# Performance work log

Hardware: AMD Instinct MI355X
Metric: run time of the kernel (lower is better)

The kernel has to match this reference:

```python
import jax, jax.numpy as jnp
import numpy as np

N_NODES = 50000
N_EDGES = 800000
F_IN = 128
HIDDEN = 96
N_CLASS = 40


def setup_inputs() -> dict:
    key = jax.random.key(0)
    ks = jax.random.split(key, 16)
    x = jax.random.normal(ks[0], (N_NODES, F_IN), dtype=jnp.float32)
    edge_index = jax.random.randint(ks[1], (2, N_EDGES), 0, N_NODES, dtype=jnp.int64)
    edge_weight = jax.random.uniform(ks[2], (N_EDGES,), dtype=jnp.float32)
    s = 0.1
    return {
        "x": x,
        "edge_index": edge_index,
        "edge_weight": edge_weight,
        "W_conv1": jax.random.normal(ks[3], (F_IN, HIDDEN), dtype=jnp.float32) * s,
        "b_conv1": jnp.zeros((HIDDEN,), dtype=jnp.float32),
        "W_conv2": jax.random.normal(ks[4], (HIDDEN, HIDDEN), dtype=jnp.float32) * s,
        "b_conv2": jnp.zeros((HIDDEN,), dtype=jnp.float32),
        "W_conv3": jax.random.normal(ks[5], (HIDDEN, HIDDEN), dtype=jnp.float32) * s,
        "b_conv3": jnp.zeros((HIDDEN,), dtype=jnp.float32),
        "W_lin1": jax.random.normal(ks[6], (F_IN, HIDDEN), dtype=jnp.float32) * s,
        "b_lin1": jnp.zeros((HIDDEN,), dtype=jnp.float32),
        "W_lin2": jax.random.normal(ks[7], (HIDDEN, N_CLASS), dtype=jnp.float32) * s,
        "b_lin2": jnp.zeros((N_CLASS,), dtype=jnp.float32),
    }


def _gcn_norm(edge_index, edge_weight, num_nodes):
    # PyG gcn_norm: add self-loops (weight 1), symmetric deg^-1/2 normalization.
    row, col = edge_index[0], edge_index[1]
    loop = jnp.arange(num_nodes, dtype=edge_index.dtype)
    rows = jnp.concatenate([row, loop])
    cols = jnp.concatenate([col, loop])
    w = jnp.concatenate([edge_weight, jnp.ones((num_nodes,), edge_weight.dtype)])
    deg = jax.ops.segment_sum(w, cols, num_segments=num_nodes)
    dinv = jnp.where(deg > 0, jax.lax.rsqrt(deg), 0.0)
    norm = dinv[rows] * w * dinv[cols]  # [E + N]
    return rows, cols, norm


def _gcn_conv(x, rows, cols, norm, W, b, num_nodes):
    h = x @ W                                   # [N, H]
    msg = norm[:, None] * h[rows]               # gather + scale, [E+N, H]
    out = jax.ops.segment_sum(msg, cols, num_segments=num_nodes)  # scatter-add
    return out + b


def reference(x, edge_index, edge_weight, W_conv1, b_conv1, W_conv2, b_conv2,
              W_conv3, b_conv3, W_lin1, b_lin1, W_lin2, b_lin2):
    N = x.shape[0]
    rows, cols, norm = _gcn_norm(edge_index, edge_weight, N)
    # x1 = elu(conv1(x)); residual branch through first_lin + stacked convs
    x1 = jax.nn.elu(_gcn_conv(x, rows, cols, norm, W_conv1, b_conv1, N))
    h = jax.nn.elu(x @ W_lin1 + b_lin1)
    # dropout p=0.5 is identity in eval mode
    h = jax.nn.elu(_gcn_conv(h, rows, cols, norm, W_conv2, b_conv2, N))
    h = jax.nn.elu(_gcn_conv(h, rows, cols, norm, W_conv3, b_conv3, N))
    h = x1 + h
    logits = h @ W_lin2 + b_lin2
    return jax.nn.log_softmax(logits, axis=-1)
```

## Files before the change

kernel.cpp:

```cpp
#include <hip/hip_runtime.h>
#include <hip/hip_bf16.h>

static __device__ __forceinline__ float elu_f(float x) {
    return x > 0.f ? x : expm1f(x);
}

static __device__ __forceinline__ ushort f2bf(float x) {
    __hip_bfloat16 h = __float2bfloat16(x);
    ushort u;
    __builtin_memcpy(&u, &h, 2);
    return u;
}

typedef short bf16x8 __attribute__((ext_vector_type(8)));
typedef float f32x4  __attribute__((ext_vector_type(4)));

static __device__ __forceinline__ void bf8_unpack(uint4 v, float* f) {
    f[0] = __uint_as_float(v.x << 16);
    f[1] = __uint_as_float(v.x & 0xffff0000u);
    f[2] = __uint_as_float(v.y << 16);
    f[3] = __uint_as_float(v.y & 0xffff0000u);
    f[4] = __uint_as_float(v.z << 16);
    f[5] = __uint_as_float(v.z & 0xffff0000u);
    f[6] = __uint_as_float(v.w << 16);
    f[7] = __uint_as_float(v.w & 0xffff0000u);
}

static __device__ __forceinline__ uint4 bf8_pack(const float* a) {
    uint4 o;
    o.x = (uint)f2bf(a[0]) | ((uint)f2bf(a[1]) << 16);
    o.y = (uint)f2bf(a[2]) | ((uint)f2bf(a[3]) << 16);
    o.z = (uint)f2bf(a[4]) | ((uint)f2bf(a[5]) << 16);
    o.w = (uint)f2bf(a[6]) | ((uint)f2bf(a[7]) << 16);
    return o;
}

__global__ void k_wprep4(const float* __restrict__ W1, const float* __restrict__ W2,
                         const float* __restrict__ W3, const float* __restrict__ W4,
                         ushort* __restrict__ T1, ushort* __restrict__ T2,
                         ushort* __restrict__ T3, ushort* __restrict__ T4,
                         int* __restrict__ bcnt) {
    const int b = blockIdx.x;
    if (b == 0) bcnt[threadIdx.x] = 0;
    const float* W; ushort* T; int K, base;
    if      (b < 48)  { W = W1; T = T1; K = 128; base = b;       }
    else if (b < 96)  { W = W2; T = T2; K = 128; base = b - 48;  }
    else if (b < 132) { W = W3; T = T3; K = 96;  base = b - 96;  }
    else              { W = W4; T = T4; K = 96;  base = b - 132; }
    const int i = base * 256 + threadIdx.x;
    const int kk = i / 96, c = i - kk * 96;
    T[c * K + kk] = f2bf(W[i]);
}

__global__ __launch_bounds__(256) void
k_bcount(const int* __restrict__ col, int* __restrict__ bcnt, int E, int bspan) {
    __shared__ int h[256];
    const int tid = threadIdx.x;
    h[tid] = 0;
    __syncthreads();
    const int e0 = blockIdx.x * 4096;
    #pragma unroll
    for (int j = 0; j < 16; ++j) {
        int e = e0 + j * 256 + tid;
        if (e < E) atomicAdd(&h[col[e] / bspan], 1);
    }
    __syncthreads();
    if (h[tid] > 0) atomicAdd(&bcnt[tid], h[tid]);
}

__global__ __launch_bounds__(256) void
k_bscan(const int* __restrict__ bcnt, int* __restrict__ bOff, int* __restrict__ bCur) {
    __shared__ int wsum[4];
    const int tid = threadIdx.x, lane = tid & 63, wid = tid >> 6;
    int v = bcnt[tid];
    int s = v;
    #pragma unroll
    for (int d = 1; d < 64; d <<= 1) {
        int t = __shfl_up(s, d);
        if (lane >= d) s += t;
    }
    if (lane == 63) wsum[wid] = s;
    __syncthreads();
    int wb = 0;
    #pragma unroll
    for (int k = 0; k < 3; ++k) if (k < wid) wb += wsum[k];
    int excl = s - v + wb;
    bOff[tid] = excl;
    bCur[tid] = excl;
    if (tid == 255) bOff[256] = excl + v;
}

__global__ __launch_bounds__(256) void
k_bscatter(const int* __restrict__ row, const int* __restrict__ col,
           const float* __restrict__ w, int* __restrict__ bCur,
           int2* __restrict__ ebuf, int* __restrict__ edst, int E, int bspan) {
    __shared__ int h[256];
    __shared__ int base[256];
    const int tid = threadIdx.x;
    h[tid] = 0;
    __syncthreads();
    const int e0 = blockIdx.x * 4096;
    int bk[16], rk[16];
    #pragma unroll
    for (int j = 0; j < 16; ++j) {
        int e = e0 + j * 256 + tid;
        if (e < E) {
            int b = col[e] / bspan;
            bk[j] = b;
            rk[j] = atomicAdd(&h[b], 1);
        }
    }
    __syncthreads();
    base[tid] = (h[tid] > 0) ? atomicAdd(&bCur[tid], h[tid]) : 0;
    __syncthreads();
    #pragma unroll
    for (int j = 0; j < 16; ++j) {
        int e = e0 + j * 256 + tid;
        if (e < E) {
            int pos = base[bk[j]] + rk[j];
            ebuf[pos] = make_int2(row[e], __float_as_int(w[e]));
            edst[pos] = col[e];
        }
    }
}

__global__ __launch_bounds__(256) void
k_csrify(const int2* __restrict__ ebuf, const int* __restrict__ edst,
         const int* __restrict__ bOff, int* __restrict__ off, float* __restrict__ dinv,
         int2* __restrict__ pairs, int N, int E, int bspan) {
    __shared__ int hist[256];
    __shared__ float degs[256];
    __shared__ int curl[256];
    __shared__ int wsum[4];
    const int tid = threadIdx.x, b = blockIdx.x;
    const int base = b * bspan;
    const int lnodes = (N - base < bspan) ? (N - base) : bspan;
    if (b == 0 && tid == 0) off[N] = E;
    if (lnodes <= 0) return;
    hist[tid] = 0;
    degs[tid] = 0.f;
    __syncthreads();
    const int e0 = bOff[b], e1 = bOff[b + 1];
    for (int e = e0 + tid; e < e1; e += 256) {
        int d = edst[e] - base;
        atomicAdd(&hist[d], 1);
        atomicAdd(&degs[d], __int_as_float(ebuf[e].y));
    }
    __syncthreads();
    const int lane = tid & 63, wid = tid >> 6;
    int v = hist[tid];
    int s = v;
    #pragma unroll
    for (int d = 1; d < 64; d <<= 1) {
        int t = __shfl_up(s, d);
        if (lane >= d) s += t;
    }
    if (lane == 63) wsum[wid] = s;
    __syncthreads();
    int wb = 0;
    #pragma unroll
    for (int k = 0; k < 3; ++k) if (k < wid) wb += wsum[k];
    int excl = s - v + wb;
    if (tid < lnodes) {
        off[base + tid] = e0 + excl;
        dinv[base + tid] = rsqrtf(1.0f + degs[tid]);
    }
    curl[tid] = excl;
    __syncthreads();
    for (int e = e0 + tid; e < e1; e += 256) {
        int d = edst[e] - base;
        int p = atomicAdd(&curl[d], 1);
        pairs[e0 + p] = ebuf[e];
    }
}

template<int K, int XBF>
__global__ __launch_bounds__(256) void
k_gemm_mfma(const void* __restrict__ Xv, const ushort* __restrict__ Wt,
            const float* __restrict__ bias, const float* __restrict__ dscale,
            void* __restrict__ outp, int N, int act, int obf16) {
    constexpr int KP = K + 8;
    __shared__ ushort XT[64 * KP];
    __shared__ ushort WT[96 * KP];
    const int tid = threadIdx.x;
    const int n0  = blockIdx.x * 64;

    #pragma unroll
    for (int i = tid; i < 96 * K / 8; i += 256) {
        const int c = i / (K / 8), q = i - c * (K / 8);
        uint4 v = reinterpret_cast<const uint4*>(Wt)[i];
        *reinterpret_cast<uint4*>(&WT[c * KP + q * 8]) = v;
    }
    if (XBF) {
        const ushort* X = (const ushort*)Xv;
        #pragma unroll
        for (int i = tid; i < 64 * K / 8; i += 256) {
            const int row = i / (K / 8), q = i - row * (K / 8);
            const int n = (n0 + row < N) ? (n0 + row) : (N - 1);
            uint4 v = *reinterpret_cast<const uint4*>(X + (size_t)n * K + q * 8);
            *reinterpret_cast<uint4*>(&XT[row * KP + q * 8]) = v;
        }
    } else {
        const float* X = (const float*)Xv;
        #pragma unroll
        for (int i = tid; i < 64 * K / 4; i += 256) {
            const int row = i / (K / 4), q = i - row * (K / 4);
            const int n = (n0 + row < N) ? (n0 + row) : (N - 1);
            float4 v = *reinterpret_cast<const float4*>(X + (size_t)n * K + q * 4);
            uint lo = (uint)f2bf(v.x) | ((uint)f2bf(v.y) << 16);
            uint hi = (uint)f2bf(v.z) | ((uint)f2bf(v.w) << 16);
            *reinterpret_cast<uint2*>(&XT[row * KP + q * 4]) = make_uint2(lo, hi);
        }
    }
    __syncthreads();

    const int lane = tid & 63;
    const int wv   = tid >> 6;
    const int r16  = lane & 15;
    const int kh   = lane >> 4;

    bf16x8 a[K / 32];
    const ushort* xbase = &XT[(wv * 16 + r16) * KP + kh * 8];
    #pragma unroll
    for (int ks = 0; ks < K / 32; ++ks)
        a[ks] = *reinterpret_cast<const bf16x8*>(xbase + ks * 32);

    f32x4 acc[6];
    #pragma unroll
    for (int ct = 0; ct < 6; ++ct) {
        f32x4 c = {0.f, 0.f, 0.f, 0.f};
        const ushort* wbase = &WT[(ct * 16 + r16) * KP + kh * 8];
        #pragma unroll
        for (int ks = 0; ks < K / 32; ++ks) {
            bf16x8 bfr = *reinterpret_cast<const bf16x8*>(wbase + ks * 32);
            c = __builtin_amdgcn_mfma_f32_16x16x32_bf16(a[ks], bfr, c, 0, 0, 0);
        }
        acc[ct] = c;
    }

    #pragma unroll
    for (int r = 0; r < 4; ++r) {
        const int n = n0 + wv * 16 + kh * 4 + r;
        if (n >= N) continue;
        const float ds = dscale ? dscale[n] : 1.f;
        #pragma unroll
        for (int ct = 0; ct < 6; ++ct) {
            const int col = ct * 16 + r16;
            float v = acc[ct][r] * ds;
            if (bias) v += bias[col];
            if (act) v = elu_f(v);
            if (obf16) ((ushort*)outp)[(size_t)n * 96 + col] = f2bf(v);
            else       ((float*)outp)[(size_t)n * 96 + col] = v;
        }
    }
}

__global__ __launch_bounds__(256) void
k_aggregate(const ushort* __restrict__ tmp, const int* __restrict__ off,
            const int2* __restrict__ pairs, const float* __restrict__ dinv,
            const float* __restrict__ bias, const ushort* __restrict__ addsrc,
            ushort* __restrict__ out, int N) {
    int t = blockIdx.x * blockDim.x + threadIdx.x;
    int n = t / 6;
    if (n >= N) return;
    const int c = (t % 6) * 16;
    const ushort* base = tmp + c;

    const float di = dinv[n];
    float f[16], acc[16];
    {
        uint4 s0 = *reinterpret_cast<const uint4*>(base + (size_t)n * 96);
        uint4 s1 = *reinterpret_cast<const uint4*>(base + (size_t)n * 96 + 8);
        bf8_unpack(s0, f);
        bf8_unpack(s1, f + 8);
        #pragma unroll
        for (int i = 0; i < 16; ++i) acc[i] = f[i];
    }

    const int e0 = off[n];
    const int e1 = off[n + 1];
    const int m  = e1 - e0;

    int2 pA, pB, pC;
    uint4 hA0, hA1, hB0, hB1, hC0, hC1;
    if (m > 0) {
        pA = pairs[e0];
        const ushort* r = base + (size_t)pA.x * 96;
        hA0 = *reinterpret_cast<const uint4*>(r);
        hA1 = *reinterpret_cast<const uint4*>(r + 8);
    }
    if (m > 1) {
        pB = pairs[e0 + 1];
        const ushort* r = base + (size_t)pB.x * 96;
        hB0 = *reinterpret_cast<const uint4*>(r);
        hB1 = *reinterpret_cast<const uint4*>(r + 8);
    }
    if (m > 2) {
        pC = pairs[e0 + 2];
        const ushort* r = base + (size_t)pC.x * 96;
        hC0 = *reinterpret_cast<const uint4*>(r);
        hC1 = *reinterpret_cast<const uint4*>(r + 8);
    }

    for (int e = e0 + 3; e < e1; ++e) {
        int2 pD = pairs[e];
        const ushort* r = base + (size_t)pD.x * 96;
        uint4 hD0 = *reinterpret_cast<const uint4*>(r);
        uint4 hD1 = *reinterpret_cast<const uint4*>(r + 8);
        float w = __int_as_float(pA.y);
        bf8_unpack(hA0, f);
        bf8_unpack(hA1, f + 8);
        #pragma unroll
        for (int i = 0; i < 16; ++i) acc[i] = fmaf(w, f[i], acc[i]);
        pA = pB; hA0 = hB0; hA1 = hB1;
        pB = pC; hB0 = hC0; hB1 = hC1;
        pC = pD; hC0 = hD0; hC1 = hD1;
    }
    if (m > 0) {
        float w = __int_as_float(pA.y);
        bf8_unpack(hA0, f); bf8_unpack(hA1, f + 8);
        #pragma unroll
        for (int i = 0; i < 16; ++i) acc[i] = fmaf(w, f[i], acc[i]);
    }
    if (m > 1) {
        float w = __int_as_float(pB.y);
        bf8_unpack(hB0, f); bf8_unpack(hB1, f + 8);
        #pragma unroll
        for (int i = 0; i < 16; ++i) acc[i] = fmaf(w, f[i], acc[i]);
    }
    if (m > 2) {
        float w = __int_as_float(pC.y);
        bf8_unpack(hC0, f); bf8_unpack(hC1, f + 8);
        #pragma unroll
        for (int i = 0; i < 16; ++i) acc[i] = fmaf(w, f[i], acc[i]);
    }

    #pragma unroll
    for (int q = 0; q < 4; ++q) {
        float4 bv = *reinterpret_cast<const float4*>(bias + c + q * 4);
        acc[q * 4 + 0] = elu_f(fmaf(di, acc[q * 4 + 0], bv.x));
        acc[q * 4 + 1] = elu_f(fmaf(di, acc[q * 4 + 1], bv.y));
        acc[q * 4 + 2] = elu_f(fmaf(di, acc[q * 4 + 2], bv.z));
        acc[q * 4 + 3] = elu_f(fmaf(di, acc[q * 4 + 3], bv.w));
    }
    if (addsrc) {
        uint4 r0 = *reinterpret_cast<const uint4*>(addsrc + (size_t)n * 96 + c);
        uint4 r1 = *reinterpret_cast<const uint4*>(addsrc + (size_t)n * 96 + c + 8);
        bf8_unpack(r0, f); bf8_unpack(r1, f + 8);
        #pragma unroll
        for (int i = 0; i < 16; ++i) acc[i] += f[i];
    }
    ushort* op = out + (size_t)n * 96 + c;
    *reinterpret_cast<uint4*>(op)     = bf8_pack(acc);
    *reinterpret_cast<uint4*>(op + 8) = bf8_pack(acc + 8);
}

__global__ __launch_bounds__(128) void
k_lin2_lsm(const ushort* __restrict__ h, const float* __restrict__ W2,
           const float* __restrict__ b2, float* __restrict__ out, int N) {
    __shared__ float hsT[96][128];
    const int tid = threadIdx.x;
    const int n0 = blockIdx.x * 128;
    const int nn = (N - n0 < 128) ? (N - n0) : 128;

    if (tid < nn) {
        const ushort* hr = h + (size_t)(n0 + tid) * 96;
        #pragma unroll
        for (int q = 0; q < 12; ++q) {
            uint4 v = *reinterpret_cast<const uint4*>(hr + q * 8);
            float f[8];
            bf8_unpack(v, f);
            #pragma unroll
            for (int j = 0; j < 8; ++j) hsT[q * 8 + j][tid] = f[j];
        }
    }
    __syncthreads();

    float acc[40];
    #pragma unroll
    for (int c = 0; c < 40; ++c) acc[c] = b2[c];
    for (int k = 0; k < 96; ++k) {
        const float hv = hsT[k][tid];
        const float* wr = W2 + k * 40;
        #pragma unroll
        for (int c = 0; c < 40; ++c) acc[c] = fmaf(hv, wr[c], acc[c]);
    }

    float m = acc[0];
    #pragma unroll
    for (int c = 1; c < 40; ++c) m = fmaxf(m, acc[c]);
    float s = 0.f;
    #pragma unroll
    for (int c = 0; c < 40; ++c) s += expf(acc[c] - m);
    const float lse = m + logf(s);

    if (tid < nn) {
        float* op = out + (size_t)(n0 + tid) * 40;
        #pragma unroll
        for (int q = 0; q < 10; ++q) {
            float4 v = make_float4(acc[q * 4 + 0] - lse, acc[q * 4 + 1] - lse,
                                   acc[q * 4 + 2] - lse, acc[q * 4 + 3] - lse);
            *reinterpret_cast<float4*>(op + q * 4) = v;
        }
    }
}


extern "C" void kernel_launch(void* const* d_in, const int* in_sizes, int n_in,
                              void* d_out, int out_size, void* d_ws, size_t ws_size,
                              hipStream_t stream) {
    const float* x   = (const float*)d_in[0];
    const int*   ei  = (const int*)d_in[1];
    const float* ew  = (const float*)d_in[2];
    const float* Wc1 = (const float*)d_in[3];
    const float* bc1 = (const float*)d_in[4];
    const float* Wc2 = (const float*)d_in[5];
    const float* bc2 = (const float*)d_in[6];
    const float* Wc3 = (const float*)d_in[7];
    const float* bc3 = (const float*)d_in[8];
    const float* Wl1 = (const float*)d_in[9];
    const float* bl1 = (const float*)d_in[10];
    const float* Wl2 = (const float*)d_in[11];
    const float* bl2 = (const float*)d_in[12];

    const int FIN = 128, HID = 96;
    const int N = in_sizes[0] / FIN;
    const int E = in_sizes[2];
    const int* row = ei;
    const int* col = ei + E;
    const int bspan = (N + 255) / 256;

    char* ws = (char*)d_ws;
    size_t o = 0;
    auto alloc = [&](size_t bytes) -> void* {
        void* p = ws + o;
        o += (bytes + 255) & ~(size_t)255;
        return p;
    };
    float*  dinv   = (float*)alloc((size_t)N * 4);
    int*    off    = (int*)  alloc((size_t)(N + 1) * 4);
    int*    bcnt   = (int*)  alloc(256 * 4);
    int*    bOff   = (int*)  alloc(257 * 4);
    int*    bCur   = (int*)  alloc(256 * 4);
    int2*   pairs  = (int2*) alloc((size_t)E * 8);
    ushort* M1     = (ushort*)alloc((size_t)N * HID * 2);
    ushort* M2     = (ushort*)alloc((size_t)N * HID * 2);
    ushort* Bb     = (ushort*)alloc((size_t)N * HID * 2);
    ushort* Cb     = (ushort*)alloc((size_t)N * HID * 2);
    ushort* Wt_c1  = (ushort*)alloc(96 * 128 * 2);
    ushort* Wt_l1  = (ushort*)alloc(96 * 128 * 2);
    ushort* Wt_c2  = (ushort*)alloc(96 * 96 * 2);
    ushort* Wt_c3  = (ushort*)alloc(96 * 96 * 2);
    int2*   ebuf   = (int2*)M1;
    int*    edst   = (int*)M2;

    const int gBkt  = (E + 4095) / 4096;
    const int nGemm = (N + 63) / 64;
    const int nAgg  = (N * 6 + 255) / 256;

    k_wprep4<<<168, 256, 0, stream>>>(Wc1, Wl1, Wc2, Wc3, Wt_c1, Wt_l1, Wt_c2, Wt_c3, bcnt);

    k_bcount<<<gBkt, 256, 0, stream>>>(col, bcnt, E, bspan);
    k_bscan<<<1, 256, 0, stream>>>(bcnt, bOff, bCur);
    k_bscatter<<<gBkt, 256, 0, stream>>>(row, col, ew, bCur, ebuf, edst, E, bspan);
    k_csrify<<<256, 256, 0, stream>>>(ebuf, edst, bOff, off, dinv, pairs, N, E, bspan);

    k_gemm_mfma<128, 0><<<nGemm, 256, 0, stream>>>(x, Wt_c1, nullptr, dinv, M1, N, 0, 1);
    k_gemm_mfma<128, 0><<<nGemm, 256, 0, stream>>>(x, Wt_l1, bl1, nullptr, Cb, N, 1, 1);

    k_aggregate<<<nAgg, 256, 0, stream>>>(M1, off, pairs, dinv, bc1, nullptr, Bb, N);

    k_gemm_mfma<96, 1><<<nGemm, 256, 0, stream>>>(Cb, Wt_c2, nullptr, dinv, M2, N, 0, 1);
    k_aggregate<<<nAgg, 256, 0, stream>>>(M2, off, pairs, dinv, bc2, nullptr, Cb, N);

    k_gemm_mfma<96, 1><<<nGemm, 256, 0, stream>>>(Cb, Wt_c3, nullptr, dinv, M1, N, 0, 1);
    k_aggregate<<<nAgg, 256, 0, stream>>>(M1, off, pairs, dinv, bc3, Bb, Cb, N);

    k_lin2_lsm<<<(N + 127) / 128, 128, 0, stream>>>(Cb, Wl2, bl2, (float*)d_out, N);
}
```

Measured before the change: 229.6 us.

## Fold bucket scan into scatter/csrify, fuse first-layer GEMMs, stage edge pairs in LDS

```diff
diff --git a/kernel.cpp b/kernel.cpp
--- a/kernel.cpp
+++ b/kernel.cpp
@@ -39,9 +39,10 @@
                          const float* __restrict__ W3, const float* __restrict__ W4,
                          ushort* __restrict__ T1, ushort* __restrict__ T2,
                          ushort* __restrict__ T3, ushort* __restrict__ T4,
-                         int* __restrict__ bcnt) {
+                         int* __restrict__ bcnt, int* __restrict__ bRes) {
     const int b = blockIdx.x;
     if (b == 0) bcnt[threadIdx.x] = 0;
+    if (b == 1) bRes[threadIdx.x] = 0;
     const float* W; ushort* T; int K, base;
     if      (b < 48)  { W = W1; T = T1; K = 128; base = b;       }
     else if (b < 96)  { W = W2; T = T2; K = 128; base = b - 48;  }
@@ -69,35 +70,17 @@
 }
 
 __global__ __launch_bounds__(256) void
-k_bscan(const int* __restrict__ bcnt, int* __restrict__ bOff, int* __restrict__ bCur) {
+k_bscatter(const int* __restrict__ row, const int* __restrict__ col,
+           const float* __restrict__ w, const int* __restrict__ bcnt,
+           int* __restrict__ bRes, int2* __restrict__ ebuf, int* __restrict__ edst,
+           int E, int bspan) {
+    __shared__ int h[256];
+    __shared__ int base[256];
+    __shared__ int sOff[256];
     __shared__ int wsum[4];
     const int tid = threadIdx.x, lane = tid & 63, wid = tid >> 6;
-    int v = bcnt[tid];
-    int s = v;
-    #pragma unroll
-    for (int d = 1; d < 64; d <<= 1) {
-        int t = __shfl_up(s, d);
-        if (lane >= d) s += t;
-    }
-    if (lane == 63) wsum[wid] = s;
-    __syncthreads();
-    int wb = 0;
-    #pragma unroll
-    for (int k = 0; k < 3; ++k) if (k < wid) wb += wsum[k];
-    int excl = s - v + wb;
-    bOff[tid] = excl;
-    bCur[tid] = excl;
-    if (tid == 255) bOff[256] = excl + v;
-}
-
-__global__ __launch_bounds__(256) void
-k_bscatter(const int* __restrict__ row, const int* __restrict__ col,
-           const float* __restrict__ w, int* __restrict__ bCur,
-           int2* __restrict__ ebuf, int* __restrict__ edst, int E, int bspan) {
-    __shared__ int h[256];
-    __shared__ int base[256];
-    const int tid = threadIdx.x;
     h[tid] = 0;
+    const int bc = bcnt[tid];
     __syncthreads();
     const int e0 = blockIdx.x * 4096;
     int bk[16], rk[16];
@@ -110,8 +93,22 @@
             rk[j] = atomicAdd(&h[b], 1);
         }
     }
-    __syncthreads();
-    base[tid] = (h[tid] > 0) ? atomicAdd(&bCur[tid], h[tid]) : 0;
+    {
+        int s = bc;
+        #pragma unroll
+        for (int d = 1; d < 64; d <<= 1) {
+            int t = __shfl_up(s, d);
+            if (lane >= d) s += t;
+        }
+        if (lane == 63) wsum[wid] = s;
+        __syncthreads();
+        int wb = 0;
+        #pragma unroll
+        for (int k = 0; k < 3; ++k) if (k < wid) wb += wsum[k];
+        sOff[tid] = s - bc + wb;
+    }
+    __syncthreads();
+    base[tid] = (h[tid] > 0) ? (sOff[tid] + atomicAdd(&bRes[tid], h[tid])) : 0;
     __syncthreads();
     #pragma unroll
     for (int j = 0; j < 16; ++j) {
@@ -126,28 +123,44 @@
 
 __global__ __launch_bounds__(256) void
 k_csrify(const int2* __restrict__ ebuf, const int* __restrict__ edst,
-         const int* __restrict__ bOff, int* __restrict__ off, float* __restrict__ dinv,
+         const int* __restrict__ bcnt, int* __restrict__ off, float* __restrict__ dinv,
          int2* __restrict__ pairs, int N, int E, int bspan) {
     __shared__ int hist[256];
     __shared__ float degs[256];
     __shared__ int curl[256];
     __shared__ int wsum[4];
+    __shared__ int sE0;
     const int tid = threadIdx.x, b = blockIdx.x;
+    const int lane = tid & 63, wid = tid >> 6;
     const int base = b * bspan;
     const int lnodes = (N - base < bspan) ? (N - base) : bspan;
     if (b == 0 && tid == 0) off[N] = E;
     if (lnodes <= 0) return;
     hist[tid] = 0;
     degs[tid] = 0.f;
-    __syncthreads();
-    const int e0 = bOff[b], e1 = bOff[b + 1];
+    const int bc = bcnt[tid];
+    {
+        int s = bc;
+        #pragma unroll
+        for (int d = 1; d < 64; d <<= 1) {
+            int t = __shfl_up(s, d);
+            if (lane >= d) s += t;
+        }
+        if (lane == 63) wsum[wid] = s;
+        __syncthreads();
+        int wb = 0;
+        #pragma unroll
+        for (int k = 0; k < 3; ++k) if (k < wid) wb += wsum[k];
+        if (tid == b) sE0 = s - bc + wb;
+    }
+    __syncthreads();
+    const int e0 = sE0, e1 = sE0 + bcnt[b];
     for (int e = e0 + tid; e < e1; e += 256) {
         int d = edst[e] - base;
         atomicAdd(&hist[d], 1);
         atomicAdd(&degs[d], __int_as_float(ebuf[e].y));
     }
     __syncthreads();
-    const int lane = tid & 63, wid = tid >> 6;
     int v = hist[tid];
     int s = v;
     #pragma unroll
@@ -175,15 +188,15 @@
 }
 
 template<int K, int XBF>
-__global__ __launch_bounds__(256) void
-k_gemm_mfma(const void* __restrict__ Xv, const ushort* __restrict__ Wt,
-            const float* __restrict__ bias, const float* __restrict__ dscale,
-            void* __restrict__ outp, int N, int act, int obf16) {
+__device__ __forceinline__ void gemm_body(
+    const void* __restrict__ Xv, const ushort* __restrict__ Wt,
+    const float* __restrict__ bias, const float* __restrict__ dscale,
+    void* __restrict__ outp, int N, int act, int obf16, int bid) {
     constexpr int KP = K + 8;
     __shared__ ushort XT[64 * KP];
     __shared__ ushort WT[96 * KP];
     const int tid = threadIdx.x;
-    const int n0  = blockIdx.x * 64;
+    const int n0  = bid * 64;
 
     #pragma unroll
     for (int i = tid; i < 96 * K / 8; i += 256) {
@@ -256,15 +269,58 @@
 }
 
 __global__ __launch_bounds__(256) void
+k_gemm_mfma96(const ushort* __restrict__ X, const ushort* __restrict__ Wt,
+              const float* __restrict__ dscale, void* __restrict__ outp, int N) {
+    gemm_body<96, 1>(X, Wt, nullptr, dscale, outp, N, 0, 1, blockIdx.x);
+}
+
+__global__ __launch_bounds__(256) void
+k_gemm_fin_dual(const float* __restrict__ X,
+                const ushort* __restrict__ Wt1, const float* __restrict__ dscale1,
+                void* __restrict__ out1,
+                const ushort* __restrict__ Wt2, const float* __restrict__ bias2,
+                void* __restrict__ out2, int N, int nHalf) {
+    if ((int)blockIdx.x < nHalf)
+        gemm_body<128, 0>(X, Wt1, nullptr, dscale1, out1, N, 0, 1, blockIdx.x);
+    else
+        gemm_body<128, 0>(X, Wt2, bias2, nullptr, out2, N, 1, 1, blockIdx.x - nHalf);
+}
+
+#define AGG_CAP 2048
+
+__global__ __launch_bounds__(256) void
 k_aggregate(const ushort* __restrict__ tmp, const int* __restrict__ off,
             const int2* __restrict__ pairs, const float* __restrict__ dinv,
             const float* __restrict__ bias, const ushort* __restrict__ addsrc,
             ushort* __restrict__ out, int N) {
-    int t = blockIdx.x * blockDim.x + threadIdx.x;
-    int n = t / 6;
+    __shared__ int2 eP[AGG_CAP];
+    __shared__ int sFlag;
+    const int tid = threadIdx.x;
+    const int t0  = blockIdx.x * 256;
+    int n_first = t0 / 6;
+    if (n_first >= N) return;
+    int n_last = (t0 + 255) / 6;
+    if (n_last >= N) n_last = N - 1;
+    const int eb0 = off[n_first];
+    const int eb1 = off[n_last + 1];
+    const int tot = eb1 - eb0;
+    if (tot <= AGG_CAP) {
+        for (int i = tid; i < tot; i += 256) eP[i] = pairs[eb0 + i];
+        if (tid == 0) sFlag = 1;
+    } else {
+        if (tid == 0) sFlag = 0;
+    }
+    __syncthreads();
+    const bool lds = (sFlag != 0);
+
+    const int n = (t0 + tid) / 6;
     if (n >= N) return;
-    const int c = (t % 6) * 16;
+    const int c = ((t0 + tid) % 6) * 16;
     const ushort* base = tmp + c;
+
+    auto LOADP = [&](int e) -> int2 {
+        return lds ? eP[e - eb0] : pairs[e];
+    };
 
     const float di = dinv[n];
     float f[16], acc[16];
@@ -284,26 +340,26 @@
     int2 pA, pB, pC;
     uint4 hA0, hA1, hB0, hB1, hC0, hC1;
     if (m > 0) {
-        pA = pairs[e0];
+        pA = LOADP(e0);
         const ushort* r = base + (size_t)pA.x * 96;
         hA0 = *reinterpret_cast<const uint4*>(r);
         hA1 = *reinterpret_cast<const uint4*>(r + 8);
     }
     if (m > 1) {
-        pB = pairs[e0 + 1];
+        pB = LOADP(e0 + 1);
         const ushort* r = base + (size_t)pB.x * 96;
         hB0 = *reinterpret_cast<const uint4*>(r);
         hB1 = *reinterpret_cast<const uint4*>(r + 8);
     }
     if (m > 2) {
-        pC = pairs[e0 + 2];
+        pC = LOADP(e0 + 2);
         const ushort* r = base + (size_t)pC.x * 96;
         hC0 = *reinterpret_cast<const uint4*>(r);
         hC1 = *reinterpret_cast<const uint4*>(r + 8);
     }
 
     for (int e = e0 + 3; e < e1; ++e) {
-        int2 pD = pairs[e];
+        int2 pD = LOADP(e);
         const ushort* r = base + (size_t)pD.x * 96;
         uint4 hD0 = *reinterpret_cast<const uint4*>(r);
         uint4 hD1 = *reinterpret_cast<const uint4*>(r + 8);
@@ -440,8 +496,7 @@
     float*  dinv   = (float*)alloc((size_t)N * 4);
     int*    off    = (int*)  alloc((size_t)(N + 1) * 4);
     int*    bcnt   = (int*)  alloc(256 * 4);
-    int*    bOff   = (int*)  alloc(257 * 4);
-    int*    bCur   = (int*)  alloc(256 * 4);
+    int*    bRes   = (int*)  alloc(256 * 4);
     int2*   pairs  = (int2*) alloc((size_t)E * 8);
     ushort* M1     = (ushort*)alloc((size_t)N * HID * 2);
     ushort* M2     = (ushort*)alloc((size_t)N * HID * 2);
@@ -458,22 +513,22 @@
     const int nGemm = (N + 63) / 64;
     const int nAgg  = (N * 6 + 255) / 256;
 
-    k_wprep4<<<168, 256, 0, stream>>>(Wc1, Wl1, Wc2, Wc3, Wt_c1, Wt_l1, Wt_c2, Wt_c3, bcnt);
+    k_wprep4<<<168, 256, 0, stream>>>(Wc1, Wl1, Wc2, Wc3, Wt_c1, Wt_l1, Wt_c2, Wt_c3,
+                                      bcnt, bRes);
 
     k_bcount<<<gBkt, 256, 0, stream>>>(col, bcnt, E, bspan);
-    k_bscan<<<1, 256, 0, stream>>>(bcnt, bOff, bCur);
-    k_bscatter<<<gBkt, 256, 0, stream>>>(row, col, ew, bCur, ebuf, edst, E, bspan);
-    k_csrify<<<256, 256, 0, stream>>>(ebuf, edst, bOff, off, dinv, pairs, N, E, bspan);
-
-    k_gemm_mfma<128, 0><<<nGemm, 256, 0, stream>>>(x, Wt_c1, nullptr, dinv, M1, N, 0, 1);
-    k_gemm_mfma<128, 0><<<nGemm, 256, 0, stream>>>(x, Wt_l1, bl1, nullptr, Cb, N, 1, 1);
+    k_bscatter<<<gBkt, 256, 0, stream>>>(row, col, ew, bcnt, bRes, ebuf, edst, E, bspan);
+    k_csrify<<<256, 256, 0, stream>>>(ebuf, edst, bcnt, off, dinv, pairs, N, E, bspan);
+
+    k_gemm_fin_dual<<<2 * nGemm, 256, 0, stream>>>(x, Wt_c1, dinv, M1,
+                                                   Wt_l1, bl1, Cb, N, nGemm);
 
     k_aggregate<<<nAgg, 256, 0, stream>>>(M1, off, pairs, dinv, bc1, nullptr, Bb, N);
 
-    k_gemm_mfma<96, 1><<<nGemm, 256, 0, stream>>>(Cb, Wt_c2, nullptr, dinv, M2, N, 0, 1);
+    k_gemm_mfma96<<<nGemm, 256, 0, stream>>>(Cb, Wt_c2, dinv, M2, N);
     k_aggregate<<<nAgg, 256, 0, stream>>>(M2, off, pairs, dinv, bc2, nullptr, Cb, N);
 
-    k_gemm_mfma<96, 1><<<nGemm, 256, 0, stream>>>(Cb, Wt_c3, nullptr, dinv, M1, N, 0, 1);
+    k_gemm_mfma96<<<nGemm, 256, 0, stream>>>(Cb, Wt_c3, dinv, M1, N);
     k_aggregate<<<nAgg, 256, 0, stream>>>(M1, off, pairs, dinv, bc3, Bb, Cb, N);
 
     k_lin2_lsm<<<(N + 127) / 128, 128, 0, stream>>>(Cb, Wl2, bl2, (float*)d_out, N);
```

Result: faster. 209.5 us (-8.7%).
